# Kernel tuning notes

Hardware: AMD Instinct MI355X
Metric: run time of the kernel (lower is better)

The kernel has to match this reference:

```python
import jax, jax.numpy as jnp
import numpy as np

B, NX, NR, D, H = 8, 512, 512, 256, 256


def setup_inputs() -> dict:
    key = jax.random.key(0)
    ks = jax.random.split(key, 8)
    s = 1.0 / np.sqrt(D)
    sh = 1.0 / np.sqrt(H)
    return {
        "X": jax.random.normal(ks[0], (B, NX, D), dtype=jnp.float32),
        "ref": jax.random.normal(ks[1], (B, NR, D), dtype=jnp.float32),
        "W_X": jax.random.normal(ks[2], (H, D), dtype=jnp.float32) * s,
        "b_X": jax.random.normal(ks[3], (H,), dtype=jnp.float32) * s,
        "W_ref": jax.random.normal(ks[4], (H, D), dtype=jnp.float32) * s,
        "b_ref": jax.random.normal(ks[5], (H,), dtype=jnp.float32) * s,
        "v_w": jax.random.normal(ks[6], (1, H), dtype=jnp.float32) * sh,
        "v_b": jax.random.normal(ks[7], (1,), dtype=jnp.float32) * sh,
    }


def reference(X, ref, W_X, b_X, W_ref, b_ref, v_w, v_b):
    # linear projections: [B, nX, H], [B, nR, H]
    hX = jnp.einsum('bxd,hd->bxh', X, W_X) + b_X
    hR = jnp.einsum('brd,hd->brh', ref, W_ref) + b_ref
    # additive (Bahdanau) scores: [B, nX, nR]
    t = jnp.tanh(hX[:, :, None, :] + hR[:, None, :, :])
    out = jnp.einsum('bxrh,h->bxr', t, v_w[0]) + v_b[0]
    # softmax over the n_X axis (dim=1 in torch)
    attn = jax.nn.softmax(out, axis=1)
    # weighted sum of X per ref position: [B, nR, D]
    weighted_X = jnp.einsum('bxe,bxr->bre', X, attn)
    return weighted_X
```

## Files before the change

kernel.cpp:

```cpp
#include <hip/hip_runtime.h>
#include <math.h>

#define CB 8
#define CNX 512
#define CNR 512
#define CD 256
#define CH 256

typedef __attribute__((ext_vector_type(8))) short short8;
typedef __attribute__((ext_vector_type(4))) float f32x4;
typedef __attribute__((ext_vector_type(4))) unsigned int uint32x4;

__device__ __forceinline__ float fast_rcp(float x) {
#if __has_builtin(__builtin_amdgcn_rcpf)
  return __builtin_amdgcn_rcpf(x);
#else
  return 1.0f / x;
#endif
}
__device__ __forceinline__ float fast_exp2(float x) {
#if __has_builtin(__builtin_amdgcn_exp2f)
  return __builtin_amdgcn_exp2f(x);
#else
  return exp2f(x);
#endif
}

__device__ __forceinline__ void split8(float4 u, float4 v, short8* H, short8* L) {
  unsigned ux = __float_as_uint(u.x), uy = __float_as_uint(u.y);
  unsigned uz = __float_as_uint(u.z), uw = __float_as_uint(u.w);
  unsigned vx = __float_as_uint(v.x), vy = __float_as_uint(v.y);
  unsigned vz = __float_as_uint(v.z), vw = __float_as_uint(v.w);
  uint32x4 Hp = {(ux >> 16) | (uy & 0xFFFF0000u),
                 (uz >> 16) | (uw & 0xFFFF0000u),
                 (vx >> 16) | (vy & 0xFFFF0000u),
                 (vz >> 16) | (vw & 0xFFFF0000u)};
  float rux = u.x - __uint_as_float(ux & 0xFFFF0000u);
  float ruy = u.y - __uint_as_float(uy & 0xFFFF0000u);
  float ruz = u.z - __uint_as_float(uz & 0xFFFF0000u);
  float ruw = u.w - __uint_as_float(uw & 0xFFFF0000u);
  float rvx = v.x - __uint_as_float(vx & 0xFFFF0000u);
  float rvy = v.y - __uint_as_float(vy & 0xFFFF0000u);
  float rvz = v.z - __uint_as_float(vz & 0xFFFF0000u);
  float rvw = v.w - __uint_as_float(vw & 0xFFFF0000u);
  uint32x4 Lp = {(__float_as_uint(rux) >> 16) | (__float_as_uint(ruy) & 0xFFFF0000u),
                 (__float_as_uint(ruz) >> 16) | (__float_as_uint(ruw) & 0xFFFF0000u),
                 (__float_as_uint(rvx) >> 16) | (__float_as_uint(rvy) & 0xFFFF0000u),
                 (__float_as_uint(rvz) >> 16) | (__float_as_uint(rvw) & 0xFFFF0000u)};
  *H = __builtin_bit_cast(short8, Hp);
  *L = __builtin_bit_cast(short8, Lp);
}

__device__ __forceinline__ void split4(float4 v, ushort4* H, ushort4* L) {
  unsigned ux = __float_as_uint(v.x), uy = __float_as_uint(v.y);
  unsigned uz = __float_as_uint(v.z), uw = __float_as_uint(v.w);
  H->x = (unsigned short)(ux >> 16);
  H->y = (unsigned short)(uy >> 16);
  H->z = (unsigned short)(uz >> 16);
  H->w = (unsigned short)(uw >> 16);
  float rx = v.x - __uint_as_float(ux & 0xFFFF0000u);
  float ry = v.y - __uint_as_float(uy & 0xFFFF0000u);
  float rz = v.z - __uint_as_float(uz & 0xFFFF0000u);
  float rw = v.w - __uint_as_float(uw & 0xFFFF0000u);
  L->x = (unsigned short)(__float_as_uint(rx) >> 16);
  L->y = (unsigned short)(__float_as_uint(ry) >> 16);
  L->z = (unsigned short)(__float_as_uint(rz) >> 16);
  L->w = (unsigned short)(__float_as_uint(rw) >> 16);
}

__global__ __launch_bounds__(256) void proj_mfma(
    const float* __restrict__ A0, const float* __restrict__ A1,
    const float* __restrict__ W0, const float* __restrict__ W1,
    const float* __restrict__ bias0, const float* __restrict__ bias1,
    float* __restrict__ E0, float* __restrict__ E1) {
  int z = blockIdx.z;
  const float* A = z ? A1 : A0;
  const float* W = z ? W1 : W0;
  const float* bias = z ? bias1 : bias0;
  float* ET = z ? E1 : E0;
  int m0 = blockIdx.x * 64, n0 = blockIdx.y * 64;
  int tid = threadIdx.x;
  int lane = tid & 63, w = tid >> 6;
  int wm = w >> 1, wn = w & 1;
  int q = lane >> 4, ml = lane & 15;
  const float* pA = A + (size_t)(m0 + wm * 32 + ml) * CD + q * 8;
  const float* pW = W + (size_t)(n0 + wn * 32 + ml) * CD + q * 8;
  f32x4 acc[2][2] = {};
  float4 ca0 = *(const float4*)(pA);
  float4 ca1 = *(const float4*)(pA + 4);
  float4 cb0 = *(const float4*)(pA + 16 * CD);
  float4 cb1 = *(const float4*)(pA + 16 * CD + 4);
  float4 cw0 = *(const float4*)(pW);
  float4 cw1 = *(const float4*)(pW + 4);
  float4 cx0 = *(const float4*)(pW + 16 * CD);
  float4 cx1 = *(const float4*)(pW + 16 * CD + 4);
  for (int s = 0; s < 8; s++) {
    float4 na0, na1, nb0, nb1, nw0, nw1, nx0, nx1;
    if (s < 7) {
      int kt = (s + 1) * 32;
      na0 = *(const float4*)(pA + kt);
      na1 = *(const float4*)(pA + kt + 4);
      nb0 = *(const float4*)(pA + 16 * CD + kt);
      nb1 = *(const float4*)(pA + 16 * CD + kt + 4);
      nw0 = *(const float4*)(pW + kt);
      nw1 = *(const float4*)(pW + kt + 4);
      nx0 = *(const float4*)(pW + 16 * CD + kt);
      nx1 = *(const float4*)(pW + 16 * CD + kt + 4);
    }
    short8 ah0, al0, ah1, al1, bh0, bl0, bh1, bl1;
    split8(ca0, ca1, &ah0, &al0);
    split8(cb0, cb1, &ah1, &al1);
    split8(cw0, cw1, &bh0, &bl0);
    split8(cx0, cx1, &bh1, &bl1);
    acc[0][0] = __builtin_amdgcn_mfma_f32_16x16x32_bf16(ah0, bh0, acc[0][0], 0, 0, 0);
    acc[0][1] = __builtin_amdgcn_mfma_f32_16x16x32_bf16(ah0, bh1, acc[0][1], 0, 0, 0);
    acc[1][0] = __builtin_amdgcn_mfma_f32_16x16x32_bf16(ah1, bh0, acc[1][0], 0, 0, 0);
    acc[1][1] = __builtin_amdgcn_mfma_f32_16x16x32_bf16(ah1, bh1, acc[1][1], 0, 0, 0);
    acc[0][0] = __builtin_amdgcn_mfma_f32_16x16x32_bf16(ah0, bl0, acc[0][0], 0, 0, 0);
    acc[0][1] = __builtin_amdgcn_mfma_f32_16x16x32_bf16(ah0, bl1, acc[0][1], 0, 0, 0);
    acc[1][0] = __builtin_amdgcn_mfma_f32_16x16x32_bf16(ah1, bl0, acc[1][0], 0, 0, 0);
    acc[1][1] = __builtin_amdgcn_mfma_f32_16x16x32_bf16(ah1, bl1, acc[1][1], 0, 0, 0);
    acc[0][0] = __builtin_amdgcn_mfma_f32_16x16x32_bf16(al0, bh0, acc[0][0], 0, 0, 0);
    acc[0][1] = __builtin_amdgcn_mfma_f32_16x16x32_bf16(al0, bh1, acc[0][1], 0, 0, 0);
    acc[1][0] = __builtin_amdgcn_mfma_f32_16x16x32_bf16(al1, bh0, acc[1][0], 0, 0, 0);
    acc[1][1] = __builtin_amdgcn_mfma_f32_16x16x32_bf16(al1, bh1, acc[1][1], 0, 0, 0);
    if (s < 7) {
      ca0 = na0; ca1 = na1; cb0 = nb0; cb1 = nb1;
      cw0 = nw0; cw1 = nw1; cx0 = nx0; cx1 = nx1;
    }
  }
  const float K2L = 2.8853900817779268f;
  int b = m0 >> 9;
  int xq = (m0 & 511) + wm * 32 + q * 4;
#pragma unroll
  for (int mi = 0; mi < 2; mi++) {
#pragma unroll
    for (int ni = 0; ni < 2; ni++) {
      int h = n0 + wn * 32 + ni * 16 + ml;
      float bb = bias[h];
      f32x4 a = acc[mi][ni];
      float4 o = {fast_exp2(K2L * (a[0] + bb)), fast_exp2(K2L * (a[1] + bb)),
                  fast_exp2(K2L * (a[2] + bb)), fast_exp2(K2L * (a[3] + bb))};
      *(float4*)(ET + ((size_t)b * CH + h) * CNX + xq + mi * 16) = o;
    }
  }
}

__global__ __launch_bounds__(512) void scores_kernel(
    const float* __restrict__ exT, const float* __restrict__ erT,
    const float* __restrict__ v_w, float* __restrict__ scT) {
  __shared__ float smem[4 * 2048 + 256];
  int b = blockIdx.z;
  int x0 = blockIdx.x * 64, r0 = blockIdx.y * 64;
  int tid = threadIdx.x;
  int g = tid >> 8;
  int t = tid & 255;
  float* xs = smem + g * 4096;
  float* rs = xs + 2048;
  float* vsh = smem + 8192;
  if (tid < 256) vsh[tid] = v_w[tid];
  int tx = t & 15, ty = t >> 4;
  int sr = t >> 4, sc = (t & 15) * 4;
  int wrot = (tid >> 6) & 7;
  const float* pX = exT + (size_t)b * CH * CNX + x0 + sc;
  const float* pR = erT + (size_t)b * CH * CNR + r0 + sc;
  int hb = g * 32;
  float4 xa0 = *(const float4*)(pX + (size_t)(hb + sr) * CNX);
  float4 xa1 = *(const float4*)(pX + (size_t)(hb + sr + 16) * CNX);
  float4 ra0 = *(const float4*)(pR + (size_t)(hb + sr) * CNR);
  float4 ra1 = *(const float4*)(pR + (size_t)(hb + sr + 16) * CNR);
  float acc[4][4] = {};
  for (int hc = hb; hc < CH; hc += 64) {
    __syncthreads();
    *(float4*)&xs[sr * 64 + sc] = xa0;
    *(float4*)&xs[(sr + 16) * 64 + sc] = xa1;
    *(float4*)&rs[sr * 64 + sc] = ra0;
    *(float4*)&rs[(sr + 16) * 64 + sc] = ra1;
    __syncthreads();
    if (hc + 64 < CH) {
      xa0 = *(const float4*)(pX + (size_t)(hc + 64 + sr) * CNX);
      xa1 = *(const float4*)(pX + (size_t)(hc + 64 + sr + 16) * CNX);
      ra0 = *(const float4*)(pR + (size_t)(hc + 64 + sr) * CNR);
      ra1 = *(const float4*)(pR + (size_t)(hc + 64 + sr + 16) * CNR);
    }
#pragma unroll 2
    for (int hq = 0; hq < 8; hq++) {
      int h0 = ((hq + wrot) & 7) * 4;
      float4 vv = *(const float4*)&vsh[hc + h0];
      float4 xv0 = *(const float4*)&xs[(h0 + 0) * 64 + tx * 4];
      float4 xv1 = *(const float4*)&xs[(h0 + 1) * 64 + tx * 4];
      float4 xv2 = *(const float4*)&xs[(h0 + 2) * 64 + tx * 4];
      float4 xv3 = *(const float4*)&xs[(h0 + 3) * 64 + tx * 4];
      float4 rv0 = *(const float4*)&rs[(h0 + 0) * 64 + ty * 4];
      float4 rv1 = *(const float4*)&rs[(h0 + 1) * 64 + ty * 4];
      float4 rv2 = *(const float4*)&rs[(h0 + 2) * 64 + ty * 4];
      float4 rv3 = *(const float4*)&rs[(h0 + 3) * 64 + ty * 4];
      float xm0[4] = {xv0.x, xv0.y, xv0.z, xv0.w};
      float xm1[4] = {xv1.x, xv1.y, xv1.z, xv1.w};
      float xm2[4] = {xv2.x, xv2.y, xv2.z, xv2.w};
      float xm3[4] = {xv3.x, xv3.y, xv3.z, xv3.w};
      float rm0[4] = {rv0.x, rv0.y, rv0.z, rv0.w};
      float rm1[4] = {rv1.x, rv1.y, rv1.z, rv1.w};
      float rm2[4] = {rv2.x, rv2.y, rv2.z, rv2.w};
      float rm3[4] = {rv3.x, rv3.y, rv3.z, rv3.w};
#pragma unroll
      for (int i = 0; i < 4; i++)
#pragma unroll
        for (int j = 0; j < 4; j++) {
          float a = fmaf(rm0[i], xm0[j], 1.0f);
          float bb = fmaf(rm1[i], xm1[j], 1.0f);
          float c = fmaf(rm2[i], xm2[j], 1.0f);
          float d = fmaf(rm3[i], xm3[j], 1.0f);
          float q12 = a * bb, q34 = c * d;
          float p12 = fmaf(vv.y, a, vv.x * bb);
          float p34 = fmaf(vv.w, c, vv.z * d);
          float num = fmaf(p34, q12, p12 * q34);
          acc[i][j] = fmaf(num, fast_rcp(q12 * q34), acc[i][j]);
        }
    }
  }
  __syncthreads();
  float* mg = smem;
  if (g == 1) {
#pragma unroll
    for (int i = 0; i < 4; i++)
#pragma unroll
      for (int j = 0; j < 4; j++)
        mg[t + 256 * (i * 4 + j)] = acc[i][j];
  }
  __syncthreads();
  if (g == 0) {
    float* pO = scT + ((size_t)b * CNR + r0 + ty * 4) * CNX + x0 + tx * 4;
#pragma unroll
    for (int i = 0; i < 4; i++) {
      float4 o = {-2.0f * (acc[i][0] + mg[t + 256 * (i * 4 + 0)]),
                  -2.0f * (acc[i][1] + mg[t + 256 * (i * 4 + 1)]),
                  -2.0f * (acc[i][2] + mg[t + 256 * (i * 4 + 2)]),
                  -2.0f * (acc[i][3] + mg[t + 256 * (i * 4 + 3)])};
      *(float4*)(pO + (size_t)i * CNX) = o;
    }
  }
}

__global__ __launch_bounds__(512) void wsum_mfma(
    const float* __restrict__ scT, const float* __restrict__ X,
    float* __restrict__ out) {
  __shared__ unsigned short lds[2][2][64][64];
  __shared__ float dn[64];
  const float L2E = 1.4426950408889634f;
  int b = blockIdx.z;
  int r0 = blockIdx.x * 64, d0 = blockIdx.y * 64;
  int tid = threadIdx.x;
  int lane = tid & 63, w = tid >> 6;
  int wm = w >> 2, wn = w & 3;
  int pr = tid >> 3, pxk = (tid & 7) * 4;
  int psl = pxk >> 3, pof = pxk & 7;
  int xd = tid & 63, xx = (tid >> 6) * 4;
  int xsl = xx >> 3, xof = xx & 7;
  const float* pS = scT + ((size_t)b * CNR + r0 + pr) * CNX + pxk;
  const float* pX = X + ((size_t)b * CNX + xx) * CD + d0 + xd;
  f32x4 acc0 = {}, acc1 = {};
  float dsum = 0.0f;
  float4 sv = *(const float4*)(pS);
  float4 xv = {pX[0], pX[CD], pX[2 * CD], pX[3 * CD]};
  {
    float4 ev = {fast_exp2(sv.x * L2E), fast_exp2(sv.y * L2E),
                 fast_exp2(sv.z * L2E), fast_exp2(sv.w * L2E)};
    dsum += (ev.x + ev.y) + (ev.z + ev.w);
    ushort4 H, L;
    split4(ev, &H, &L);
    unsigned short* rp = &lds[0][0][pr][0];
    *(ushort4*)(rp + ((psl ^ (pr & 7)) << 3) + pof) = H;
    *(ushort4*)(rp + (((psl + 4) ^ (pr & 7)) << 3) + pof) = L;
    split4(xv, &H, &L);
    unsigned short* rx = &lds[0][1][xd][0];
    *(ushort4*)(rx + ((xsl ^ (xd & 7)) << 3) + xof) = H;
    *(ushort4*)(rx + (((xsl + 4) ^ (xd & 7)) << 3) + xof) = L;
  }
  int q = lane >> 4;
  int mr0 = wm * 32 + (lane & 15);
  int mr1 = mr0 + 16;
  int nr = wn * 16 + (lane & 15);
  for (int s = 0; s < 16; s++) {
    __syncthreads();
    if (s < 15) {
      int kt = (s + 1) * 32;
      sv = *(const float4*)(pS + kt);
      xv.x = pX[(size_t)(kt + 0) * CD];
      xv.y = pX[(size_t)(kt + 1) * CD];
      xv.z = pX[(size_t)(kt + 2) * CD];
      xv.w = pX[(size_t)(kt + 3) * CD];
    }
    int cur = s & 1;
    const unsigned short* Pt = &lds[cur][0][0][0];
    const unsigned short* Xt = &lds[cur][1][0][0];
    short8 ah0 = *(const short8*)(Pt + mr0 * 64 + ((q ^ (mr0 & 7)) << 3));
    short8 al0 = *(const short8*)(Pt + mr0 * 64 + (((q + 4) ^ (mr0 & 7)) << 3));
    short8 ah1 = *(const short8*)(Pt + mr1 * 64 + ((q ^ (mr1 & 7)) << 3));
    short8 al1 = *(const short8*)(Pt + mr1 * 64 + (((q + 4) ^ (mr1 & 7)) << 3));
    short8 bh = *(const short8*)(Xt + nr * 64 + ((q ^ (nr & 7)) << 3));
    short8 bl = *(const short8*)(Xt + nr * 64 + (((q + 4) ^ (nr & 7)) << 3));
    acc0 = __builtin_amdgcn_mfma_f32_16x16x32_bf16(ah0, bh, acc0, 0, 0, 0);
    acc1 = __builtin_amdgcn_mfma_f32_16x16x32_bf16(ah1, bh, acc1, 0, 0, 0);
    acc0 = __builtin_amdgcn_mfma_f32_16x16x32_bf16(ah0, bl, acc0, 0, 0, 0);
    acc1 = __builtin_amdgcn_mfma_f32_16x16x32_bf16(ah1, bl, acc1, 0, 0, 0);
    acc0 = __builtin_amdgcn_mfma_f32_16x16x32_bf16(al0, bh, acc0, 0, 0, 0);
    acc1 = __builtin_amdgcn_mfma_f32_16x16x32_bf16(al1, bh, acc1, 0, 0, 0);
    if (s < 15) {
      int nxt = cur ^ 1;
      float4 ev = {fast_exp2(sv.x * L2E), fast_exp2(sv.y * L2E),
                   fast_exp2(sv.z * L2E), fast_exp2(sv.w * L2E)};
      dsum += (ev.x + ev.y) + (ev.z + ev.w);
      ushort4 H, L;
      split4(ev, &H, &L);
      unsigned short* rp = &lds[nxt][0][pr][0];
      *(ushort4*)(rp + ((psl ^ (pr & 7)) << 3) + pof) = H;
      *(ushort4*)(rp + (((psl + 4) ^ (pr & 7)) << 3) + pof) = L;
      split4(xv, &H, &L);
      unsigned short* rx = &lds[nxt][1][xd][0];
      *(ushort4*)(rx + ((xsl ^ (xd & 7)) << 3) + xof) = H;
      *(ushort4*)(rx + (((xsl + 4) ^ (xd & 7)) << 3) + xof) = L;
    }
  }
  dsum += __shfl_xor(dsum, 1, 64);
  dsum += __shfl_xor(dsum, 2, 64);
  dsum += __shfl_xor(dsum, 4, 64);
  if ((tid & 7) == 0) dn[pr] = dsum;
  __syncthreads();
  int col = d0 + wn * 16 + (lane & 15);
  float* pO = out + ((size_t)b * CNR + r0) * CD + col;
#pragma unroll
  for (int j = 0; j < 4; j++) {
    int row = wm * 32 + q * 4 + j;
    pO[(size_t)row * CD] = acc0[j] * fast_rcp(dn[row]);
  }
#pragma unroll
  for (int j = 0; j < 4; j++) {
    int row = wm * 32 + 16 + q * 4 + j;
    pO[(size_t)row * CD] = acc1[j] * fast_rcp(dn[row]);
  }
}

extern "C" void kernel_launch(void* const* d_in, const int* in_sizes, int n_in,
                              void* d_out, int out_size, void* d_ws, size_t ws_size,
                              hipStream_t stream) {
  const float* X     = (const float*)d_in[0];
  const float* ref   = (const float*)d_in[1];
  const float* W_X   = (const float*)d_in[2];
  const float* b_X   = (const float*)d_in[3];
  const float* W_ref = (const float*)d_in[4];
  const float* b_ref = (const float*)d_in[5];
  const float* v_w   = (const float*)d_in[6];
  float* out = (float*)d_out;
  float* ws  = (float*)d_ws;

  float* exT = ws;
  float* erT = ws + 1048576;
  float* scT = ws + 2097152;

  proj_mfma<<<dim3(64, 4, 2), 256, 0, stream>>>(X, ref, W_X, W_ref, b_X, b_ref, exT, erT);
  scores_kernel<<<dim3(8, 8, 8), 512, 0, stream>>>(exT, erT, v_w, scT);
  wsum_mfma<<<dim3(8, 4, 8), 512, 0, stream>>>(scT, X, out);
}
```

Measured before the change: 142.0 us.

## Stage projection GEMM tiles through LDS with async global_load_lds double buffering

Projection kernel operands are no longer loaded straight into registers. Each k-step's A and W tiles are now copied into a double-buffered, XOR-swizzled shared-memory tile using global_load_lds, and every wave reads its fragments from LDS. This removes duplicate global loads across waves that share rows and makes the next tile's prefetch asynchronous, at the cost of a barrier every iteration and extra LDS traffic. It only touches the projection kernel, which is a small part of the total work next to the scores kernel.

```diff
diff --git a/kernel.cpp b/kernel.cpp
--- a/kernel.cpp
+++ b/kernel.cpp
@@ -24,6 +24,12 @@
 #else
   return exp2f(x);
 #endif
+}
+
+__device__ __forceinline__ void gload_lds16(const float* g, float* l) {
+  __builtin_amdgcn_global_load_lds(
+      (const __attribute__((address_space(1))) unsigned int*)g,
+      (__attribute__((address_space(3))) unsigned int*)l, 16, 0, 0);
 }
 
 __device__ __forceinline__ void split8(float4 u, float4 v, short8* H, short8* L) {
@@ -73,6 +79,7 @@
     const float* __restrict__ W0, const float* __restrict__ W1,
     const float* __restrict__ bias0, const float* __restrict__ bias1,
     float* __restrict__ E0, float* __restrict__ E1) {
+  __shared__ float lds[2][2][64 * 32];
   int z = blockIdx.z;
   const float* A = z ? A1 : A0;
   const float* W = z ? W1 : W0;
@@ -83,35 +90,48 @@
   int lane = tid & 63, w = tid >> 6;
   int wm = w >> 1, wn = w & 1;
   int q = lane >> 4, ml = lane & 15;
-  const float* pA = A + (size_t)(m0 + wm * 32 + ml) * CD + q * 8;
-  const float* pW = W + (size_t)(n0 + wn * 32 + ml) * CD + q * 8;
+  int crow = lane >> 3, cslot = lane & 7;
+  int gslot = (cslot ^ crow) << 2;
+  float* dA = &lds[0][0][0];
+  int c0 = w * 4;
+  auto STAGE = [&](int buf, int kt) {
+#pragma unroll
+    for (int cc = 0; cc < 4; cc++) {
+      int c = c0 + cc;
+      int mat = c >> 3;
+      int r8 = (c & 7) * 8;
+      const float* base = mat ? W + (size_t)(n0 + r8 + crow) * CD
+                              : A + (size_t)(m0 + r8 + crow) * CD;
+      gload_lds16(base + kt + gslot, &lds[buf][mat][r8 * 32]);
+    }
+  };
   f32x4 acc[2][2] = {};
-  float4 ca0 = *(const float4*)(pA);
-  float4 ca1 = *(const float4*)(pA + 4);
-  float4 cb0 = *(const float4*)(pA + 16 * CD);
-  float4 cb1 = *(const float4*)(pA + 16 * CD + 4);
-  float4 cw0 = *(const float4*)(pW);
-  float4 cw1 = *(const float4*)(pW + 4);
-  float4 cx0 = *(const float4*)(pW + 16 * CD);
-  float4 cx1 = *(const float4*)(pW + 16 * CD + 4);
+  STAGE(0, 0);
+  int arow = wm * 32 + ml;
+  int brow = wn * 32 + ml;
   for (int s = 0; s < 8; s++) {
-    float4 na0, na1, nb0, nb1, nw0, nw1, nx0, nx1;
-    if (s < 7) {
-      int kt = (s + 1) * 32;
-      na0 = *(const float4*)(pA + kt);
-      na1 = *(const float4*)(pA + kt + 4);
-      nb0 = *(const float4*)(pA + 16 * CD + kt);
-      nb1 = *(const float4*)(pA + 16 * CD + kt + 4);
-      nw0 = *(const float4*)(pW + kt);
-      nw1 = *(const float4*)(pW + kt + 4);
-      nx0 = *(const float4*)(pW + 16 * CD + kt);
-      nx1 = *(const float4*)(pW + 16 * CD + kt + 4);
-    }
+    __syncthreads();
+    int cur = s & 1;
+    if (s < 7) STAGE(cur ^ 1, (s + 1) * 32);
+    const float* Ab0 = &lds[cur][0][arow * 32];
+    const float* Ab1 = &lds[cur][0][(arow + 16) * 32];
+    const float* Wb0 = &lds[cur][1][brow * 32];
+    const float* Wb1 = &lds[cur][1][(brow + 16) * 32];
+    int sa0 = ((2 * q) ^ (arow & 7)) * 4, sa1 = ((2 * q + 1) ^ (arow & 7)) * 4;
+    int sb0 = ((2 * q) ^ (brow & 7)) * 4, sb1 = ((2 * q + 1) ^ (brow & 7)) * 4;
+    float4 fa0 = *(const float4*)(Ab0 + sa0);
+    float4 fa1 = *(const float4*)(Ab0 + sa1);
+    float4 fb0 = *(const float4*)(Ab1 + sa0);
+    float4 fb1 = *(const float4*)(Ab1 + sa1);
+    float4 fw0 = *(const float4*)(Wb0 + sb0);
+    float4 fw1 = *(const float4*)(Wb0 + sb1);
+    float4 fx0 = *(const float4*)(Wb1 + sb0);
+    float4 fx1 = *(const float4*)(Wb1 + sb1);
     short8 ah0, al0, ah1, al1, bh0, bl0, bh1, bl1;
-    split8(ca0, ca1, &ah0, &al0);
-    split8(cb0, cb1, &ah1, &al1);
-    split8(cw0, cw1, &bh0, &bl0);
-    split8(cx0, cx1, &bh1, &bl1);
+    split8(fa0, fa1, &ah0, &al0);
+    split8(fb0, fb1, &ah1, &al1);
+    split8(fw0, fw1, &bh0, &bl0);
+    split8(fx0, fx1, &bh1, &bl1);
     acc[0][0] = __builtin_amdgcn_mfma_f32_16x16x32_bf16(ah0, bh0, acc[0][0], 0, 0, 0);
     acc[0][1] = __builtin_amdgcn_mfma_f32_16x16x32_bf16(ah0, bh1, acc[0][1], 0, 0, 0);
     acc[1][0] = __builtin_amdgcn_mfma_f32_16x16x32_bf16(ah1, bh0, acc[1][0], 0, 0, 0);
@@ -124,11 +144,8 @@
     acc[0][1] = __builtin_amdgcn_mfma_f32_16x16x32_bf16(al0, bh1, acc[0][1], 0, 0, 0);
     acc[1][0] = __builtin_amdgcn_mfma_f32_16x16x32_bf16(al1, bh0, acc[1][0], 0, 0, 0);
     acc[1][1] = __builtin_amdgcn_mfma_f32_16x16x32_bf16(al1, bh1, acc[1][1], 0, 0, 0);
-    if (s < 7) {
-      ca0 = na0; ca1 = na1; cb0 = nb0; cb1 = nb1;
-      cw0 = nw0; cw1 = nw1; cx0 = nx0; cx1 = nx1;
-    }
-  }
+  }
+  (void)dA;
   const float K2L = 2.8853900817779268f;
   int b = m0 >> 9;
   int xq = (m0 & 511) + wm * 32 + q * 4;
```

Measured after the change: 135.7 us. 4.5% less time.
